# Performance work log

Hardware: AMD Instinct MI355X
Metric: run time of the kernel (lower is better)

## Reference

```python
import jax, jax.numpy as jnp
import numpy as np

EPS = 1e-12  # torch F.normalize eps
NUM_HEADS = 4
DT = 0.25
NUM_STEPS = 4


def _l2norm(x, axis=-1):
    n = jnp.sqrt(jnp.sum(x * x, axis=axis, keepdims=True))
    return x / jnp.maximum(n, EPS)


def setup_inputs() -> dict:
    key = jax.random.key(0)
    k0, k1, k2, k3, k4 = jax.random.split(key, 5)
    B, T, D = 4, 2048, 256
    z = jax.random.normal(k0, (B, T, D), dtype=jnp.float32)
    omega = jax.random.normal(k1, (1, 1, D), dtype=jnp.float32) * 0.1
    Wqk = jax.random.normal(k2, (2 * D, D), dtype=jnp.float32) * (1.0 / np.sqrt(D))
    Wout = jax.random.normal(k3, (D, D), dtype=jnp.float32) * (1.0 / np.sqrt(D))
    bout = jax.random.normal(k4, (D,), dtype=jnp.float32) * 0.01
    return {"z": z, "omega": omega, "Wqk": Wqk, "Wout": Wout, "bout": bout}


def _kuramoto(x, omega, Wqk, Wout, bout):
    # x: [B, T, D]
    B, T, D = x.shape
    hd = D // NUM_HEADS
    qk = x @ Wqk.T  # [B, T, 2D]
    q, k = jnp.split(qk, 2, axis=-1)
    q = _l2norm(q.reshape(B, T, NUM_HEADS, hd))  # cosine-normalized per head
    k = _l2norm(k.reshape(B, T, NUM_HEADS, hd))
    # coupling: [B, H, T, T] cosine similarity
    coupling = jnp.einsum("bqhd,bkhd->bhqk", q, k)
    # sin nonlinearity replaces softmax
    force = jnp.einsum("bhqk,bkhd->bqhd", jnp.sin(coupling), k).reshape(B, T, D)
    return omega + force @ Wout.T + bout


def reference(z, omega, Wqk, Wout, bout):
    def f(x):
        return _kuramoto(x, omega, Wqk, Wout, bout)

    x = z
    for _ in range(NUM_STEPS):
        x = _l2norm(x)
        k1 = f(x)
        k2 = f(x + DT / 2 * k1)
        k3 = f(x + DT / 2 * k2)
        k4 = f(x + DT * k3)
        x = x + DT / 6 * (k1 + 2 * k2 + 2 * k3 + k4)
    return _l2norm(x)
```

## Files before the change

### kernel.cpp

```cpp
#include <hip/hip_runtime.h>
#include <cmath>

#define NB 4
#define TT 2048
#define DD 256
#define NH 4
#define BT (NB*TT)

static constexpr float DT_ = 0.25f;

typedef _Float16 f16x8 __attribute__((ext_vector_type(8)));
typedef _Float16 f16x4 __attribute__((ext_vector_type(4)));
typedef float    f32x4 __attribute__((ext_vector_type(4)));

static constexpr size_t HSZ = (size_t)NB * NH * TT * 64;
static constexpr size_t FSZ = (size_t)BT * 256;

__global__ __launch_bounds__(256)
void split_weights(const float* __restrict__ Wqk, const float* __restrict__ Wout,
                   _Float16* __restrict__ WqkH, _Float16* __restrict__ WqkL,
                   _Float16* __restrict__ WoutH, _Float16* __restrict__ WoutL)
{
    const int idx = blockIdx.x * 256 + threadIdx.x;
    const float4 v = (idx < 32768) ? ((const float4*)Wqk)[idx]
                                   : ((const float4*)Wout)[idx - 32768];
    f16x4 h, l;
    h[0]=(_Float16)v.x; l[0]=(_Float16)(v.x-(float)h[0]);
    h[1]=(_Float16)v.y; l[1]=(_Float16)(v.y-(float)h[1]);
    h[2]=(_Float16)v.z; l[2]=(_Float16)(v.z-(float)h[2]);
    h[3]=(_Float16)v.w; l[3]=(_Float16)(v.w-(float)h[3]);
    if (idx < 32768) { ((f16x4*)WqkH)[idx] = h; ((f16x4*)WqkL)[idx] = l; }
    else { ((f16x4*)WoutH)[idx-32768] = h; ((f16x4*)WoutL)[idx-32768] = l; }
}

__global__ __launch_bounds__(256)
void l2norm_rows(const float* __restrict__ src, float* __restrict__ dst,
                 _Float16* __restrict__ dstH, _Float16* __restrict__ dstL) {
    const int wave = threadIdx.x >> 6;
    const int lane = threadIdx.x & 63;
    const size_t row = (size_t)blockIdx.x * 4 + wave;
    float4 v = ((const float4*)(src + row * DD))[lane];
    float ss = v.x*v.x + v.y*v.y + v.z*v.z + v.w*v.w;
    #pragma unroll
    for (int off = 32; off; off >>= 1) ss += __shfl_xor(ss, off, 64);
    const float inv = 1.0f / fmaxf(sqrtf(ss), 1e-12f);
    v.x *= inv; v.y *= inv; v.z *= inv; v.w *= inv;
    ((float4*)(dst + row * DD))[lane] = v;
    if (dstH != nullptr) {
        f16x4 h, l;
        h[0]=(_Float16)v.x; l[0]=(_Float16)(v.x-(float)h[0]);
        h[1]=(_Float16)v.y; l[1]=(_Float16)(v.y-(float)h[1]);
        h[2]=(_Float16)v.z; l[2]=(_Float16)(v.z-(float)h[2]);
        h[3]=(_Float16)v.w; l[3]=(_Float16)(v.w-(float)h[3]);
        ((f16x4*)(dstH + row * DD))[lane] = h;
        ((f16x4*)(dstL + row * DD))[lane] = l;
    }
}

__global__ __launch_bounds__(256)
void gemm_mfma(const _Float16* __restrict__ AH, const _Float16* __restrict__ AL,
               const float* __restrict__ Fp,
               const _Float16* __restrict__ BH, const _Float16* __restrict__ BL,
               const float* __restrict__ omega, const float* __restrict__ bout,
               const float* __restrict__ xin, float* __restrict__ kacc,
               _Float16* __restrict__ xsH, _Float16* __restrict__ xsL,
               float* __restrict__ xout,
               _Float16* __restrict__ Qhi, _Float16* __restrict__ Qlo,
               _Float16* __restrict__ Khi, _Float16* __restrict__ Klo,
               _Float16* __restrict__ KtrH,
               int stage)
{
    __shared__ _Float16 Ah[128 * 72];
    __shared__ _Float16 Al[128 * 72];
    __shared__ _Float16 Bh[64 * 72];
    __shared__ _Float16 Bl[64 * 72];
    const int m0 = blockIdx.x * 128, n0 = blockIdx.y * 64;
    const int t  = threadIdx.x;
    const int w  = t >> 6;
    const int l  = t & 63;
    const int lr = l & 15;
    const int lq = l >> 4;

    f32x4 acc[2][4];
    #pragma unroll
    for (int s = 0; s < 2; ++s)
        #pragma unroll
        for (int nt = 0; nt < 4; ++nt) acc[s][nt] = (f32x4){0.f,0.f,0.f,0.f};

    for (int kc = 0; kc < 4; ++kc) {
        const int k0 = kc * 64;
        __syncthreads();
        if (stage < 0) {
            #pragma unroll
            for (int s2 = 0; s2 < 4; ++s2) {
                const int idx = t + 256 * s2;
                const int r = idx >> 3, c8 = (idx & 7) * 8;
                *(uint4*)&Ah[r * 72 + c8] = *(const uint4*)(AH + (size_t)(m0 + r) * 256 + k0 + c8);
                *(uint4*)&Al[r * 72 + c8] = *(const uint4*)(AL + (size_t)(m0 + r) * 256 + k0 + c8);
            }
        } else {
            #pragma unroll
            for (int s2 = 0; s2 < 4; ++s2) {
                const int idx = t + 256 * s2;
                const int r = idx >> 3, c8 = (idx & 7) * 8;
                const size_t go = (size_t)(m0 + r) * 256 + k0 + c8;
                const float4 a0 = *(const float4*)(Fp + go);
                const float4 a1 = *(const float4*)(Fp + go + 4);
                const float4 b0 = *(const float4*)(Fp + FSZ + go);
                const float4 b1 = *(const float4*)(Fp + FSZ + go + 4);
                const float4 c0 = *(const float4*)(Fp + 2*FSZ + go);
                const float4 c1 = *(const float4*)(Fp + 2*FSZ + go + 4);
                const float sv[8] = {a0.x+b0.x+c0.x, a0.y+b0.y+c0.y,
                                     a0.z+b0.z+c0.z, a0.w+b0.w+c0.w,
                                     a1.x+b1.x+c1.x, a1.y+b1.y+c1.y,
                                     a1.z+b1.z+c1.z, a1.w+b1.w+c1.w};
                f16x8 hv, lv;
                #pragma unroll
                for (int e = 0; e < 8; ++e) {
                    hv[e] = (_Float16)sv[e];
                    lv[e] = (_Float16)(sv[e] - (float)hv[e]);
                }
                *(f16x8*)&Ah[r * 72 + c8] = hv;
                *(f16x8*)&Al[r * 72 + c8] = lv;
            }
        }
        #pragma unroll
        for (int s2 = 0; s2 < 2; ++s2) {
            const int idx = t + 256 * s2;
            const int r = idx >> 3, c8 = (idx & 7) * 8;
            *(uint4*)&Bh[r * 72 + c8] = *(const uint4*)(BH + (size_t)(n0 + r) * 256 + k0 + c8);
            *(uint4*)&Bl[r * 72 + c8] = *(const uint4*)(BL + (size_t)(n0 + r) * 256 + k0 + c8);
        }
        __syncthreads();
        #pragma unroll
        for (int c = 0; c < 2; ++c) {
            f16x8 ah[2], al[2], bh[4], bl[4];
            #pragma unroll
            for (int s = 0; s < 2; ++s) {
                ah[s] = *(const f16x8*)&Ah[(32*w + 16*s + lr) * 72 + 32*c + 8*lq];
                al[s] = *(const f16x8*)&Al[(32*w + 16*s + lr) * 72 + 32*c + 8*lq];
            }
            #pragma unroll
            for (int nt = 0; nt < 4; ++nt) {
                bh[nt] = *(const f16x8*)&Bh[(16*nt + lr) * 72 + 32*c + 8*lq];
                bl[nt] = *(const f16x8*)&Bl[(16*nt + lr) * 72 + 32*c + 8*lq];
            }
            #pragma unroll
            for (int s = 0; s < 2; ++s)
                #pragma unroll
                for (int nt = 0; nt < 4; ++nt) {
                    acc[s][nt] = __builtin_amdgcn_mfma_f32_16x16x32_f16(ah[s], bh[nt], acc[s][nt], 0, 0, 0);
                    acc[s][nt] = __builtin_amdgcn_mfma_f32_16x16x32_f16(ah[s], bl[nt], acc[s][nt], 0, 0, 0);
                    acc[s][nt] = __builtin_amdgcn_mfma_f32_16x16x32_f16(al[s], bh[nt], acc[s][nt], 0, 0, 0);
                }
        }
    }

    if (stage < 0) {
        float ss[2][4];
        #pragma unroll
        for (int s = 0; s < 2; ++s)
            #pragma unroll
            for (int r = 0; r < 4; ++r) {
                float v = 0.f;
                #pragma unroll
                for (int nt = 0; nt < 4; ++nt) v += acc[s][nt][r] * acc[s][nt][r];
                ss[s][r] = v;
            }
        #pragma unroll
        for (int off = 1; off < 16; off <<= 1)
            #pragma unroll
            for (int s = 0; s < 2; ++s)
                #pragma unroll
                for (int r = 0; r < 4; ++r)
                    ss[s][r] += __shfl_xor(ss[s][r], off, 64);
        const int  b    = m0 >> 11;
        const int  h    = (n0 >> 6) & 3;
        const bool is_k = (n0 >= 256);
        const size_t bhi = (size_t)b * NH + h;
        _Float16* dhi = (is_k ? Khi : Qhi) + bhi * (size_t)TT * 64;
        _Float16* dlo = (is_k ? Klo : Qlo) + bhi * (size_t)TT * 64;
        const int mloc = m0 & (TT - 1);
        #pragma unroll
        for (int s = 0; s < 2; ++s) {
            const int r0 = 32*w + 16*s + 4*lq;
            float inv[4];
            #pragma unroll
            for (int r = 0; r < 4; ++r) inv[r] = 1.0f / fmaxf(sqrtf(ss[s][r]), 1e-12f);
            #pragma unroll
            for (int nt = 0; nt < 4; ++nt) {
                const int d = 16*nt + lr;
                f16x4 hv, lv;
                #pragma unroll
                for (int r = 0; r < 4; ++r) {
                    const float val = acc[s][nt][r] * inv[r];
                    hv[r] = (_Float16)val;
                    lv[r] = (_Float16)(val - (float)hv[r]);
                    dhi[(size_t)(mloc + r0 + r) * 64 + d] = hv[r];
                    dlo[(size_t)(mloc + r0 + r) * 64 + d] = lv[r];
                }
                if (is_k) {
                    const size_t tb = bhi * (size_t)64 * TT + (size_t)d * TT + mloc + r0;
                    *(f16x4*)(KtrH + tb) = hv;
                }
            }
        }
    } else {
        #pragma unroll
        for (int s = 0; s < 2; ++s) {
            const int row0 = m0 + 32*w + 16*s + 4*lq;
            #pragma unroll
            for (int nt = 0; nt < 4; ++nt) {
                const int col = n0 + 16*nt + lr;
                const float ob = omega[col] + bout[col];
                #pragma unroll
                for (int r = 0; r < 4; ++r) {
                    const size_t off = (size_t)(row0 + r) * 256 + col;
                    const float f = acc[s][nt][r] + ob;
                    if (stage == 0) {
                        kacc[off] = f;
                        const float xv = xin[off] + 0.125f * f;
                        const _Float16 xh = (_Float16)xv;
                        xsH[off] = xh;
                        xsL[off] = (_Float16)(xv - (float)xh);
                    } else if (stage < 3) {
                        kacc[off] += 2.0f * f;
                        const float c = (stage == 1) ? 0.125f : 0.25f;
                        const float xv = xin[off] + c * f;
                        const _Float16 xh = (_Float16)xv;
                        xsH[off] = xh;
                        xsL[off] = (_Float16)(xv - (float)xh);
                    } else {
                        xout[off] = xin[off] + (DT_ / 6.0f) * (kacc[off] + f);
                    }
                }
            }
        }
    }
}

__global__ __launch_bounds__(256, 3)
void kuramoto_attn(const _Float16* __restrict__ Qhi, const _Float16* __restrict__ Qlo,
                   const _Float16* __restrict__ Khi, const _Float16* __restrict__ Klo,
                   const _Float16* __restrict__ KtrH,
                   float* __restrict__ Fp)
{
    __shared__ _Float16 KjH[64 * 72];
    __shared__ _Float16 KjL[64 * 72];
    __shared__ _Float16 KdH[64 * 72];
    __shared__ _Float16 Pw[4][2][16 * 68];
    const int bh = blockIdx.z;
    const int b  = bh >> 2, h = bh & 3;
    const size_t base  = (size_t)bh * TT * 64;
    const size_t tbase = (size_t)bh * 64 * TT;
    const int t0 = blockIdx.y * 11;
    const int tn = (blockIdx.y == 2) ? 10 : 11;
    float* Fout = Fp + (size_t)blockIdx.y * FSZ;
    const int t = threadIdx.x;
    const int w = t >> 6;
    const int l = t & 63;
    const int lr = l & 15;
    const int lq = l >> 4;
    const int i0 = blockIdx.x * 128 + w * 32;

    f16x8 qh[2][2], ql[2][2];
    #pragma unroll
    for (int s = 0; s < 2; ++s) {
        const size_t qoff = base + (size_t)(i0 + 16*s + lr) * 64 + lq * 8;
        qh[s][0] = *(const f16x8*)(Qhi + qoff);
        qh[s][1] = *(const f16x8*)(Qhi + qoff + 32);
        ql[s][0] = *(const f16x8*)(Qlo + qoff);
        ql[s][1] = *(const f16x8*)(Qlo + qoff + 32);
    }

    f32x4 Facc[2][4];
    #pragma unroll
    for (int s = 0; s < 2; ++s)
        #pragma unroll
        for (int nt = 0; nt < 4; ++nt) Facc[s][nt] = (f32x4){0.f, 0.f, 0.f, 0.f};

    const int sr = t >> 3;
    const int so = (t & 7) * 8;

    for (int tt = 0; tt < tn; ++tt) {
        const int j0 = (t0 + tt) * 64;
        __syncthreads();
        {
            *(uint4*)&KjH[sr * 72 + so]        = *(const uint4*)(Khi + base + (size_t)(j0 + sr) * 64 + so);
            *(uint4*)&KjH[(sr + 32) * 72 + so] = *(const uint4*)(Khi + base + (size_t)(j0 + sr + 32) * 64 + so);
            *(uint4*)&KjL[sr * 72 + so]        = *(const uint4*)(Klo + base + (size_t)(j0 + sr) * 64 + so);
            *(uint4*)&KjL[(sr + 32) * 72 + so] = *(const uint4*)(Klo + base + (size_t)(j0 + sr + 32) * 64 + so);
            *(uint4*)&KdH[sr * 72 + so]        = *(const uint4*)(KtrH + tbase + (size_t)sr * TT + j0 + so);
            *(uint4*)&KdH[(sr + 32) * 72 + so] = *(const uint4*)(KtrH + tbase + (size_t)(sr + 32) * TT + j0 + so);
        }
        __syncthreads();
        #pragma unroll
        for (int nt = 0; nt < 4; ++nt) {
            f16x8 kh0 = *(const f16x8*)&KjH[(16*nt + lr) * 72 + lq * 8];
            f16x8 kh1 = *(const f16x8*)&KjH[(16*nt + lr) * 72 + 32 + lq * 8];
            f16x8 kl0 = *(const f16x8*)&KjL[(16*nt + lr) * 72 + lq * 8];
            f16x8 kl1 = *(const f16x8*)&KjL[(16*nt + lr) * 72 + 32 + lq * 8];
            #pragma unroll
            for (int s = 0; s < 2; ++s) {
                f32x4 a = (f32x4){0.f, 0.f, 0.f, 0.f};
                a = __builtin_amdgcn_mfma_f32_16x16x32_f16(kh0, qh[s][0], a, 0, 0, 0);
                a = __builtin_amdgcn_mfma_f32_16x16x32_f16(kh1, qh[s][1], a, 0, 0, 0);
                a = __builtin_amdgcn_mfma_f32_16x16x32_f16(kl0, qh[s][0], a, 0, 0, 0);
                a = __builtin_amdgcn_mfma_f32_16x16x32_f16(kl1, qh[s][1], a, 0, 0, 0);
                a = __builtin_amdgcn_mfma_f32_16x16x32_f16(kh0, ql[s][0], a, 0, 0, 0);
                a = __builtin_amdgcn_mfma_f32_16x16x32_f16(kh1, ql[s][1], a, 0, 0, 0);
                f16x4 pv;
                #pragma unroll
                for (int r = 0; r < 4; ++r) pv[r] = (_Float16)__sinf(a[r]);
                *(f16x4*)&Pw[w][s][lr * 68 + 16*nt + 4*lq] = pv;
            }
        }
        f16x8 ph[2][2];
        #pragma unroll
        for (int s = 0; s < 2; ++s) {
            ph[s][0] = *(const f16x8*)&Pw[w][s][lr * 68 + lq * 8];
            ph[s][1] = *(const f16x8*)&Pw[w][s][lr * 68 + 32 + lq * 8];
        }
        #pragma unroll
        for (int nt = 0; nt < 4; ++nt) {
            f16x8 kh0 = *(const f16x8*)&KdH[(16*nt + lr) * 72 + lq * 8];
            f16x8 kh1 = *(const f16x8*)&KdH[(16*nt + lr) * 72 + 32 + lq * 8];
            #pragma unroll
            for (int s = 0; s < 2; ++s) {
                Facc[s][nt] = __builtin_amdgcn_mfma_f32_16x16x32_f16(ph[s][0], kh0, Facc[s][nt], 0, 0, 0);
                Facc[s][nt] = __builtin_amdgcn_mfma_f32_16x16x32_f16(ph[s][1], kh1, Facc[s][nt], 0, 0, 0);
            }
        }
    }
    #pragma unroll
    for (int s = 0; s < 2; ++s) {
        float* fo = Fout + ((size_t)b * TT + i0 + 16*s + 4*lq) * 256 + h * 64 + lr;
        #pragma unroll
        for (int nt = 0; nt < 4; ++nt)
            #pragma unroll
            for (int r = 0; r < 4; ++r)
                fo[(size_t)r * 256 + nt * 16] = Facc[s][nt][r];
    }
}

extern "C" void kernel_launch(void* const* d_in, const int* in_sizes, int n_in,
                              void* d_out, int out_size, void* d_ws, size_t ws_size,
                              hipStream_t stream) {
    const float* z     = (const float*)d_in[0];
    const float* omega = (const float*)d_in[1];
    const float* Wqk   = (const float*)d_in[2];
    const float* Wout  = (const float*)d_in[3];
    const float* bout  = (const float*)d_in[4];

    float* x    = (float*)d_ws;
    float* kacc = x + FSZ;
    float* Fp   = kacc + FSZ;
    _Float16* xsH  = (_Float16*)(Fp + 3 * FSZ);
    _Float16* xsL  = xsH  + FSZ;
    _Float16* Qhi  = xsL  + FSZ;
    _Float16* Qlo  = Qhi  + HSZ;
    _Float16* Khi  = Qlo  + HSZ;
    _Float16* Klo  = Khi  + HSZ;
    _Float16* KtrH = Klo  + HSZ;
    _Float16* WqkH = KtrH + HSZ;
    _Float16* WqkL = WqkH + (size_t)512 * 256;
    _Float16* WoutH= WqkL + (size_t)512 * 256;
    _Float16* WoutL= WoutH + (size_t)256 * 256;

    split_weights<<<192, 256, 0, stream>>>(Wqk, Wout, WqkH, WqkL, WoutH, WoutL);

    for (int step = 0; step < 4; ++step) {
        l2norm_rows<<<BT / 4, 256, 0, stream>>>(step == 0 ? z : x, x, xsH, xsL);
        for (int s = 0; s < 4; ++s) {
            gemm_mfma<<<dim3(BT / 128, 8), 256, 0, stream>>>(
                xsH, xsL, nullptr, WqkH, WqkL,
                nullptr, nullptr, nullptr, nullptr, nullptr, nullptr, nullptr,
                Qhi, Qlo, Khi, Klo, KtrH, -1);
            kuramoto_attn<<<dim3(TT / 128, 3, NB * NH), 256, 0, stream>>>(
                Qhi, Qlo, Khi, Klo, KtrH, Fp);
            gemm_mfma<<<dim3(BT / 128, 4), 256, 0, stream>>>(
                nullptr, nullptr, Fp, WoutH, WoutL,
                omega, bout, x, kacc, xsH, xsL, x,
                nullptr, nullptr, nullptr, nullptr, nullptr, s);
        }
    }
    l2norm_rows<<<BT / 4, 256, 0, stream>>>(x, (float*)d_out, nullptr, nullptr);
}
```

Baseline: 1.300 ms.

## Split attention keys four ways and alias P scratch onto K tiles

The attention kernel now splits the key dimension into four chunks of 512 (instead of three uneven chunks), raising grid size to 1024 blocks, and the output GEMM sums four partial force buffers. Shared memory is cut by reusing the K hi/lo tile region as the sin-probability scratch, with an extra barrier and register buffering of the sin values, and launch bounds raised to 4 blocks per CU for higher occupancy. The cost is one more partial-sum buffer read in the epilogue GEMM, an additional __syncthreads per tile, and tighter register limits that may cause spills.

After: 1.565 ms. 1.2x slower.

```diff
diff --git a/kernel.cpp b/kernel.cpp
--- a/kernel.cpp
+++ b/kernel.cpp
@@ -104,16 +104,14 @@
                 const int idx = t + 256 * s2;
                 const int r = idx >> 3, c8 = (idx & 7) * 8;
                 const size_t go = (size_t)(m0 + r) * 256 + k0 + c8;
-                const float4 a0 = *(const float4*)(Fp + go);
-                const float4 a1 = *(const float4*)(Fp + go + 4);
-                const float4 b0 = *(const float4*)(Fp + FSZ + go);
-                const float4 b1 = *(const float4*)(Fp + FSZ + go + 4);
-                const float4 c0 = *(const float4*)(Fp + 2*FSZ + go);
-                const float4 c1 = *(const float4*)(Fp + 2*FSZ + go + 4);
-                const float sv[8] = {a0.x+b0.x+c0.x, a0.y+b0.y+c0.y,
-                                     a0.z+b0.z+c0.z, a0.w+b0.w+c0.w,
-                                     a1.x+b1.x+c1.x, a1.y+b1.y+c1.y,
-                                     a1.z+b1.z+c1.z, a1.w+b1.w+c1.w};
+                float sv[8] = {0,0,0,0,0,0,0,0};
+                #pragma unroll
+                for (int p = 0; p < 4; ++p) {
+                    const float4 a0 = *(const float4*)(Fp + p*FSZ + go);
+                    const float4 a1 = *(const float4*)(Fp + p*FSZ + go + 4);
+                    sv[0]+=a0.x; sv[1]+=a0.y; sv[2]+=a0.z; sv[3]+=a0.w;
+                    sv[4]+=a1.x; sv[5]+=a1.y; sv[6]+=a1.z; sv[7]+=a1.w;
+                }
                 f16x8 hv, lv;
                 #pragma unroll
                 for (int e = 0; e < 8; ++e) {
@@ -239,22 +237,22 @@
     }
 }
 
-__global__ __launch_bounds__(256, 3)
+__global__ __launch_bounds__(256, 4)
 void kuramoto_attn(const _Float16* __restrict__ Qhi, const _Float16* __restrict__ Qlo,
                    const _Float16* __restrict__ Khi, const _Float16* __restrict__ Klo,
                    const _Float16* __restrict__ KtrH,
                    float* __restrict__ Fp)
 {
-    __shared__ _Float16 KjH[64 * 72];
-    __shared__ _Float16 KjL[64 * 72];
+    __shared__ _Float16 KA[2][64 * 72];
     __shared__ _Float16 KdH[64 * 72];
-    __shared__ _Float16 Pw[4][2][16 * 68];
+    _Float16* KjH = KA[0];
+    _Float16* KjL = KA[1];
+    _Float16* Pw  = KA[0];
     const int bh = blockIdx.z;
     const int b  = bh >> 2, h = bh & 3;
     const size_t base  = (size_t)bh * TT * 64;
     const size_t tbase = (size_t)bh * 64 * TT;
-    const int t0 = blockIdx.y * 11;
-    const int tn = (blockIdx.y == 2) ? 10 : 11;
+    const int j00 = blockIdx.y * 512;
     float* Fout = Fp + (size_t)blockIdx.y * FSZ;
     const int t = threadIdx.x;
     const int w = t >> 6;
@@ -282,8 +280,8 @@
     const int sr = t >> 3;
     const int so = (t & 7) * 8;
 
-    for (int tt = 0; tt < tn; ++tt) {
-        const int j0 = (t0 + tt) * 64;
+    for (int tt = 0; tt < 8; ++tt) {
+        const int j0 = j00 + tt * 64;
         __syncthreads();
         {
             *(uint4*)&KjH[sr * 72 + so]        = *(const uint4*)(Khi + base + (size_t)(j0 + sr) * 64 + so);
@@ -294,6 +292,7 @@
             *(uint4*)&KdH[(sr + 32) * 72 + so] = *(const uint4*)(KtrH + tbase + (size_t)(sr + 32) * TT + j0 + so);
         }
         __syncthreads();
+        f16x4 pv[2][4];
         #pragma unroll
         for (int nt = 0; nt < 4; ++nt) {
             f16x8 kh0 = *(const f16x8*)&KjH[(16*nt + lr) * 72 + lq * 8];
@@ -309,17 +308,21 @@
                 a = __builtin_amdgcn_mfma_f32_16x16x32_f16(kl1, qh[s][1], a, 0, 0, 0);
                 a = __builtin_amdgcn_mfma_f32_16x16x32_f16(kh0, ql[s][0], a, 0, 0, 0);
                 a = __builtin_amdgcn_mfma_f32_16x16x32_f16(kh1, ql[s][1], a, 0, 0, 0);
-                f16x4 pv;
-                #pragma unroll
-                for (int r = 0; r < 4; ++r) pv[r] = (_Float16)__sinf(a[r]);
-                *(f16x4*)&Pw[w][s][lr * 68 + 16*nt + 4*lq] = pv;
-            }
-        }
+                #pragma unroll
+                for (int r = 0; r < 4; ++r) pv[s][nt][r] = (_Float16)__sinf(a[r]);
+            }
+        }
+        __syncthreads();
+        #pragma unroll
+        for (int s = 0; s < 2; ++s)
+            #pragma unroll
+            for (int nt = 0; nt < 4; ++nt)
+                *(f16x4*)&Pw[(w*2 + s) * 1088 + lr * 68 + 16*nt + 4*lq] = pv[s][nt];
         f16x8 ph[2][2];
         #pragma unroll
         for (int s = 0; s < 2; ++s) {
-            ph[s][0] = *(const f16x8*)&Pw[w][s][lr * 68 + lq * 8];
-            ph[s][1] = *(const f16x8*)&Pw[w][s][lr * 68 + 32 + lq * 8];
+            ph[s][0] = *(const f16x8*)&Pw[(w*2 + s) * 1088 + lr * 68 + lq * 8];
+            ph[s][1] = *(const f16x8*)&Pw[(w*2 + s) * 1088 + lr * 68 + 32 + lq * 8];
         }
         #pragma unroll
         for (int nt = 0; nt < 4; ++nt) {
@@ -355,7 +358,7 @@
     float* x    = (float*)d_ws;
     float* kacc = x + FSZ;
     float* Fp   = kacc + FSZ;
-    _Float16* xsH  = (_Float16*)(Fp + 3 * FSZ);
+    _Float16* xsH  = (_Float16*)(Fp + 4 * FSZ);
     _Float16* xsL  = xsH  + FSZ;
     _Float16* Qhi  = xsL  + FSZ;
     _Float16* Qlo  = Qhi  + HSZ;
@@ -376,7 +379,7 @@
                 xsH, xsL, nullptr, WqkH, WqkL,
                 nullptr, nullptr, nullptr, nullptr, nullptr, nullptr, nullptr,
                 Qhi, Qlo, Khi, Klo, KtrH, -1);
-            kuramoto_attn<<<dim3(TT / 128, 3, NB * NH), 256, 0, stream>>>(
+            kuramoto_attn<<<dim3(TT / 128, 4, NB * NH), 256, 0, stream>>>(
                 Qhi, Qlo, Khi, Klo, KtrH, Fp);
             gemm_mfma<<<dim3(BT / 128, 4), 256, 0, stream>>>(
                 nullptr, nullptr, Fp, WoutH, WoutL,
```

## Fold Wout into Wqk to skip per-stage output projections in RK4

Applied to the files above, without the earlier changes.

Precomputes a combined weight Wqk·Wout and bias term so each intermediate RK4 stage computes its Q/K projection directly from the attention force plus the cached base projection of x. This removes the separate output GEMM and the split-fp16 state writes for three of the four stages. The force sum is accumulated and a single output GEMM runs at the end of each step. In exchange it adds fp32 traffic for the cached projection and accumulator, and rounds the combined weight to a split-fp16 representation.

After: 1.196 ms. 1.09x faster.

```diff
diff --git a/kernel.cpp b/kernel.cpp
--- a/kernel.cpp
+++ b/kernel.cpp
@@ -31,6 +31,32 @@
     h[3]=(_Float16)v.w; l[3]=(_Float16)(v.w-(float)h[3]);
     if (idx < 32768) { ((f16x4*)WqkH)[idx] = h; ((f16x4*)WqkL)[idx] = l; }
     else { ((f16x4*)WoutH)[idx-32768] = h; ((f16x4*)WoutL)[idx-32768] = l; }
+}
+
+__global__ __launch_bounds__(256)
+void comb_weights(const float* __restrict__ Wqk, const float* __restrict__ Wout,
+                  const float* __restrict__ omega, const float* __restrict__ bout,
+                  _Float16* __restrict__ WcombH, _Float16* __restrict__ WcombL,
+                  float* __restrict__ qkob)
+{
+    __shared__ float qrow[256];
+    __shared__ float pr[256];
+    const int n = blockIdx.x;
+    const int k = threadIdx.x;
+    qrow[k] = Wqk[n * 256 + k];
+    __syncthreads();
+    float s = 0.f;
+    for (int m = 0; m < 256; ++m) s = fmaf(qrow[m], Wout[m * 256 + k], s);
+    const _Float16 h = (_Float16)s;
+    WcombH[n * 256 + k] = h;
+    WcombL[n * 256 + k] = (_Float16)(s - (float)h);
+    pr[k] = (omega[k] + bout[k]) * qrow[k];
+    __syncthreads();
+    if (k == 0) {
+        float t = 0.f;
+        for (int i = 0; i < 256; ++i) t += pr[i];
+        qkob[n] = t;
+    }
 }
 
 __global__ __launch_bounds__(256)
@@ -59,16 +85,15 @@
 
 __global__ __launch_bounds__(256)
 void gemm_mfma(const _Float16* __restrict__ AH, const _Float16* __restrict__ AL,
-               const float* __restrict__ Fp,
+               const float* __restrict__ Fp, float* __restrict__ Facc,
                const _Float16* __restrict__ BH, const _Float16* __restrict__ BL,
+               float* __restrict__ qkx, const float* __restrict__ qkob,
                const float* __restrict__ omega, const float* __restrict__ bout,
-               const float* __restrict__ xin, float* __restrict__ kacc,
-               _Float16* __restrict__ xsH, _Float16* __restrict__ xsL,
-               float* __restrict__ xout,
+               const float* __restrict__ xin, float* __restrict__ xout,
                _Float16* __restrict__ Qhi, _Float16* __restrict__ Qlo,
                _Float16* __restrict__ Khi, _Float16* __restrict__ Klo,
                _Float16* __restrict__ KtrH,
-               int stage)
+               int mode, float cc, int faccm)
 {
     __shared__ _Float16 Ah[128 * 72];
     __shared__ _Float16 Al[128 * 72];
@@ -90,7 +115,7 @@
     for (int kc = 0; kc < 4; ++kc) {
         const int k0 = kc * 64;
         __syncthreads();
-        if (stage < 0) {
+        if (mode == 0) {
             #pragma unroll
             for (int s2 = 0; s2 < 4; ++s2) {
                 const int idx = t + 256 * s2;
@@ -104,16 +129,33 @@
                 const int idx = t + 256 * s2;
                 const int r = idx >> 3, c8 = (idx & 7) * 8;
                 const size_t go = (size_t)(m0 + r) * 256 + k0 + c8;
-                const float4 a0 = *(const float4*)(Fp + go);
-                const float4 a1 = *(const float4*)(Fp + go + 4);
-                const float4 b0 = *(const float4*)(Fp + FSZ + go);
-                const float4 b1 = *(const float4*)(Fp + FSZ + go + 4);
-                const float4 c0 = *(const float4*)(Fp + 2*FSZ + go);
-                const float4 c1 = *(const float4*)(Fp + 2*FSZ + go + 4);
-                const float sv[8] = {a0.x+b0.x+c0.x, a0.y+b0.y+c0.y,
-                                     a0.z+b0.z+c0.z, a0.w+b0.w+c0.w,
-                                     a1.x+b1.x+c1.x, a1.y+b1.y+c1.y,
-                                     a1.z+b1.z+c1.z, a1.w+b1.w+c1.w};
+                float sv[8] = {0,0,0,0,0,0,0,0};
+                if (mode == 2) {
+                    const float4 a0 = *(const float4*)(Facc + go);
+                    const float4 a1 = *(const float4*)(Facc + go + 4);
+                    sv[0]=a0.x; sv[1]=a0.y; sv[2]=a0.z; sv[3]=a0.w;
+                    sv[4]=a1.x; sv[5]=a1.y; sv[6]=a1.z; sv[7]=a1.w;
+                }
+                #pragma unroll
+                for (int p = 0; p < 3; ++p) {
+                    const float4 a0 = *(const float4*)(Fp + p*FSZ + go);
+                    const float4 a1 = *(const float4*)(Fp + p*FSZ + go + 4);
+                    sv[0]+=a0.x; sv[1]+=a0.y; sv[2]+=a0.z; sv[3]+=a0.w;
+                    sv[4]+=a1.x; sv[5]+=a1.y; sv[6]+=a1.z; sv[7]+=a1.w;
+                }
+                if (mode == 1 && blockIdx.y == 0) {
+                    if (faccm == 1) {
+                        *(float4*)(Facc + go)     = make_float4(sv[0], sv[1], sv[2], sv[3]);
+                        *(float4*)(Facc + go + 4) = make_float4(sv[4], sv[5], sv[6], sv[7]);
+                    } else {
+                        float4 f0 = *(const float4*)(Facc + go);
+                        float4 f1 = *(const float4*)(Facc + go + 4);
+                        f0.x += 2.f*sv[0]; f0.y += 2.f*sv[1]; f0.z += 2.f*sv[2]; f0.w += 2.f*sv[3];
+                        f1.x += 2.f*sv[4]; f1.y += 2.f*sv[5]; f1.z += 2.f*sv[6]; f1.w += 2.f*sv[7];
+                        *(float4*)(Facc + go)     = f0;
+                        *(float4*)(Facc + go + 4) = f1;
+                    }
+                }
                 f16x8 hv, lv;
                 #pragma unroll
                 for (int e = 0; e < 8; ++e) {
@@ -156,7 +198,41 @@
         }
     }
 
-    if (stage < 0) {
+    if (mode == 2) {
+        #pragma unroll
+        for (int s = 0; s < 2; ++s) {
+            const int row0 = m0 + 32*w + 16*s + 4*lq;
+            #pragma unroll
+            for (int nt = 0; nt < 4; ++nt) {
+                const int col = n0 + 16*nt + lr;
+                const float ob = omega[col] + bout[col];
+                #pragma unroll
+                for (int r = 0; r < 4; ++r) {
+                    const size_t off = (size_t)(row0 + r) * 256 + col;
+                    xout[off] = xin[off] + (DT_ / 6.0f) * acc[s][nt][r] + DT_ * ob;
+                }
+            }
+        }
+    } else {
+        float val[2][4][4];
+        #pragma unroll
+        for (int s = 0; s < 2; ++s) {
+            const int row0 = m0 + 32*w + 16*s + 4*lq;
+            #pragma unroll
+            for (int nt = 0; nt < 4; ++nt) {
+                const int col = n0 + 16*nt + lr;
+                #pragma unroll
+                for (int r = 0; r < 4; ++r) {
+                    const size_t qo = (size_t)(row0 + r) * 512 + col;
+                    if (mode == 0) {
+                        val[s][nt][r] = acc[s][nt][r];
+                        qkx[qo] = acc[s][nt][r];
+                    } else {
+                        val[s][nt][r] = qkx[qo] + cc * (acc[s][nt][r] + qkob[col]);
+                    }
+                }
+            }
+        }
         float ss[2][4];
         #pragma unroll
         for (int s = 0; s < 2; ++s)
@@ -164,7 +240,7 @@
             for (int r = 0; r < 4; ++r) {
                 float v = 0.f;
                 #pragma unroll
-                for (int nt = 0; nt < 4; ++nt) v += acc[s][nt][r] * acc[s][nt][r];
+                for (int nt = 0; nt < 4; ++nt) v += val[s][nt][r] * val[s][nt][r];
                 ss[s][r] = v;
             }
         #pragma unroll
@@ -193,46 +269,15 @@
                 f16x4 hv, lv;
                 #pragma unroll
                 for (int r = 0; r < 4; ++r) {
-                    const float val = acc[s][nt][r] * inv[r];
-                    hv[r] = (_Float16)val;
-                    lv[r] = (_Float16)(val - (float)hv[r]);
+                    const float v2 = val[s][nt][r] * inv[r];
+                    hv[r] = (_Float16)v2;
+                    lv[r] = (_Float16)(v2 - (float)hv[r]);
                     dhi[(size_t)(mloc + r0 + r) * 64 + d] = hv[r];
                     dlo[(size_t)(mloc + r0 + r) * 64 + d] = lv[r];
                 }
                 if (is_k) {
                     const size_t tb = bhi * (size_t)64 * TT + (size_t)d * TT + mloc + r0;
                     *(f16x4*)(KtrH + tb) = hv;
-                }
-            }
-        }
-    } else {
-        #pragma unroll
-        for (int s = 0; s < 2; ++s) {
-            const int row0 = m0 + 32*w + 16*s + 4*lq;
-            #pragma unroll
-            for (int nt = 0; nt < 4; ++nt) {
-                const int col = n0 + 16*nt + lr;
-                const float ob = omega[col] + bout[col];
-                #pragma unroll
-                for (int r = 0; r < 4; ++r) {
-                    const size_t off = (size_t)(row0 + r) * 256 + col;
-                    const float f = acc[s][nt][r] + ob;
-                    if (stage == 0) {
-                        kacc[off] = f;
-                        const float xv = xin[off] + 0.125f * f;
-                        const _Float16 xh = (_Float16)xv;
-                        xsH[off] = xh;
-                        xsL[off] = (_Float16)(xv - (float)xh);
-                    } else if (stage < 3) {
-                        kacc[off] += 2.0f * f;
-                        const float c = (stage == 1) ? 0.125f : 0.25f;
-                        const float xv = xin[off] + c * f;
-                        const _Float16 xh = (_Float16)xv;
-                        xsH[off] = xh;
-                        xsL[off] = (_Float16)(xv - (float)xh);
-                    } else {
-                        xout[off] = xin[off] + (DT_ / 6.0f) * (kacc[off] + f);
-                    }
                 }
             }
         }
@@ -353,9 +398,11 @@
     const float* bout  = (const float*)d_in[4];
 
     float* x    = (float*)d_ws;
-    float* kacc = x + FSZ;
-    float* Fp   = kacc + FSZ;
-    _Float16* xsH  = (_Float16*)(Fp + 3 * FSZ);
+    float* Facc = x + FSZ;
+    float* Fp   = Facc + FSZ;
+    float* qkx  = Fp + 3 * FSZ;
+    float* qkob = qkx + (size_t)BT * 512;
+    _Float16* xsH  = (_Float16*)(qkob + 512);
     _Float16* xsL  = xsH  + FSZ;
     _Float16* Qhi  = xsL  + FSZ;
     _Float16* Qlo  = Qhi  + HSZ;
@@ -366,23 +413,33 @@
     _Float16* WqkL = WqkH + (size_t)512 * 256;
     _Float16* WoutH= WqkL + (size_t)512 * 256;
     _Float16* WoutL= WoutH + (size_t)256 * 256;
+    _Float16* WcombH = WoutL + (size_t)256 * 256;
+    _Float16* WcombL = WcombH + (size_t)512 * 256;
 
     split_weights<<<192, 256, 0, stream>>>(Wqk, Wout, WqkH, WqkL, WoutH, WoutL);
+    comb_weights<<<512, 256, 0, stream>>>(Wqk, Wout, omega, bout, WcombH, WcombL, qkob);
 
     for (int step = 0; step < 4; ++step) {
         l2norm_rows<<<BT / 4, 256, 0, stream>>>(step == 0 ? z : x, x, xsH, xsL);
-        for (int s = 0; s < 4; ++s) {
+        gemm_mfma<<<dim3(BT / 128, 8), 256, 0, stream>>>(
+            xsH, xsL, nullptr, nullptr, WqkH, WqkL, qkx, nullptr,
+            nullptr, nullptr, nullptr, nullptr,
+            Qhi, Qlo, Khi, Klo, KtrH, 0, 0.f, 0);
+        kuramoto_attn<<<dim3(TT / 128, 3, NB * NH), 256, 0, stream>>>(
+            Qhi, Qlo, Khi, Klo, KtrH, Fp);
+        for (int s = 1; s <= 3; ++s) {
+            const float cs = (s == 3) ? 0.25f : 0.125f;
             gemm_mfma<<<dim3(BT / 128, 8), 256, 0, stream>>>(
-                xsH, xsL, nullptr, WqkH, WqkL,
-                nullptr, nullptr, nullptr, nullptr, nullptr, nullptr, nullptr,
-                Qhi, Qlo, Khi, Klo, KtrH, -1);
+                nullptr, nullptr, Fp, Facc, WcombH, WcombL, qkx, qkob,
+                nullptr, nullptr, nullptr, nullptr,
+                Qhi, Qlo, Khi, Klo, KtrH, 1, cs, (s == 1) ? 1 : 2);
             kuramoto_attn<<<dim3(TT / 128, 3, NB * NH), 256, 0, stream>>>(
                 Qhi, Qlo, Khi, Klo, KtrH, Fp);
-            gemm_mfma<<<dim3(BT / 128, 4), 256, 0, stream>>>(
-                nullptr, nullptr, Fp, WoutH, WoutL,
-                omega, bout, x, kacc, xsH, xsL, x,
-                nullptr, nullptr, nullptr, nullptr, nullptr, s);
-        }
+        }
+        gemm_mfma<<<dim3(BT / 128, 4), 256, 0, stream>>>(
+            nullptr, nullptr, Fp, Facc, WoutH, WoutL, nullptr, nullptr,
+            omega, bout, x, x,
+            nullptr, nullptr, nullptr, nullptr, nullptr, 2, 0.f, 0);
     }
     l2norm_rows<<<BT / 4, 256, 0, stream>>>(x, (float*)d_out, nullptr, nullptr);
 }
```
